# Kernel optimization log

Hardware: AMD Instinct MI355X
Metric: run time of the kernel (lower is better)

The kernel has to match this reference:

```python
import jax, jax.numpy as jnp
import numpy as np

MAX_SH_DEGREE = 3
NUM_BASES = (MAX_SH_DEGREE + 1) ** 2  # 16


def eval_sh_bases_fast(dirs):
    """SH bases up to degree 3 for unit directions [..., 3] -> [..., 16].
    Matches gsplat's _eval_sh_bases_fast constants/order."""
    x, y, z = dirs[..., 0], dirs[..., 1], dirs[..., 2]
    z2 = z * z
    fTmp0B = -1.092548430592079 * z
    fC1 = x * x - y * y
    fS1 = 2.0 * x * y
    fTmp0C = -2.285228997322329 * z2 + 0.4570457994644658
    fTmp1B = 1.445305721320277 * z
    fC2 = x * fC1 - y * fS1
    fS2 = x * fS1 + y * fC1
    ones = jnp.full_like(x, 0.2820947917738781)
    return jnp.stack([
        ones,
        -0.48860251190292 * y,
        0.48860251190292 * z,
        -0.48860251190292 * x,
        0.5462742152960395 * fS1,
        fTmp0B * y,
        0.9461746957575601 * z2 - 0.3153915652525201,
        fTmp0B * x,
        0.5462742152960395 * fC1,
        -0.5900435899266435 * fS2,
        fTmp1B * fS1,
        fTmp0C * y,
        z * (1.865881662950577 * z2 - 1.119528997770346),
        fTmp0C * x,
        fTmp1B * fC1,
        -0.5900435899266435 * fC2,
    ], axis=-1)


def setup_inputs() -> dict:
    key = jax.random.key(0)
    ks = jax.random.split(key, 10)
    C, N, F, E, W = 4, 250000, 32, 16, 128
    D_IN = E + F + NUM_BASES  # 64
    return {
        "features": jax.random.normal(ks[0], (N, F), jnp.float32),
        "dirs": jax.random.normal(ks[1], (C, N, 3), jnp.float32),
        "embed_table": jax.random.normal(ks[2], (1000, E), jnp.float32) * 0.1,
        "W0": jax.random.normal(ks[3], (D_IN, W), jnp.float32) / np.sqrt(D_IN),
        "b0": jax.random.normal(ks[4], (W,), jnp.float32) * 0.01,
        "W1": jax.random.normal(ks[5], (W, W), jnp.float32) / np.sqrt(W),
        "b1": jax.random.normal(ks[6], (W,), jnp.float32) * 0.01,
        "W2": jax.random.normal(ks[7], (W, 3), jnp.float32) / np.sqrt(W),
        "b2": jax.random.normal(ks[8], (3,), jnp.float32) * 0.01,
        "embed_ids": jax.random.randint(ks[9], (C,), 0, 1000, jnp.int64 if jax.config.jax_enable_x64 else jnp.int32),
        "sh_degree": 3,
    }


def reference(features, dirs, embed_table, W0, b0, W1, b1, W2, b2, embed_ids, sh_degree):
    C, N = dirs.shape[:2]
    E = embed_table.shape[1]
    F_dim = features.shape[1]
    # camera embeddings broadcast over splats
    emb = embed_table[embed_ids]                                   # [C, E]
    emb = jnp.broadcast_to(emb[:, None, :], (C, N, E))
    feats = jnp.broadcast_to(features[None, :, :], (C, N, F_dim))
    # F.normalize(dirs, dim=-1): divide by norm clamped at eps=1e-12
    norm = jnp.linalg.norm(dirs, axis=-1, keepdims=True)
    nd = dirs / jnp.maximum(norm, 1e-12)
    nb_use = (sh_degree + 1) ** 2  # static python int
    sh = eval_sh_bases_fast(nd)                                    # [C, N, 16]
    if nb_use < NUM_BASES:  # zero bases beyond requested degree
        mask = (jnp.arange(NUM_BASES) < nb_use).astype(sh.dtype)
        sh = sh * mask
    x = jnp.concatenate([emb, feats, sh], axis=-1)                 # [C, N, 64]
    h = jax.nn.relu(x @ W0 + b0)
    h = jax.nn.relu(h @ W1 + b1)
    return h @ W2 + b2                                             # [C, N, 3]
```

## Files before the change

kernel.cpp:

```cpp
#include <hip/hip_runtime.h>
#include <cstdint>
#include <cstddef>

typedef _Float16 half8 __attribute__((ext_vector_type(8)));
typedef __fp16 fp16x2 __attribute__((ext_vector_type(2)));
typedef float floatx16 __attribute__((ext_vector_type(16)));
typedef unsigned uint2v __attribute__((ext_vector_type(2)));


__global__ void vdc_prep_kernel(const float* __restrict__ W0,
                                const float* __restrict__ W1,
                                const float* __restrict__ W2,
                                const float* __restrict__ b0,
                                const float* __restrict__ b1,
                                const float* __restrict__ emb_tab,
                                const int* __restrict__ embed_ids,
                                int C,
                                _Float16* __restrict__ ws) {
    int i = blockIdx.x * 256 + threadIdx.x;
    int w0end   = C * 6144;
    int w1end   = w0end + 16384;
    int w2end   = w1end + 4096;
    int tailend = w2end + C * 128 + 128;
    if (i < w0end) {
        int c = i / 6144, r = i - c * 6144;
        int ci = r >> 9, l = (r >> 3) & 63, ii = r & 7;
        int mt = ci / 3, ks = ci - mt * 3;
        int j  = mt * 32 + (l & 31);
        int kk = ks * 16 + (l >> 5) * 8 + ii;
        ws[i] = (_Float16)W0[(16 + kk) * 128 + j];
    } else if (i < w1end) {
        int r = i - w0end;
        int ci = r >> 9, l = (r >> 3) & 63, ii = r & 7;
        int mt = ci >> 3, ks = ci & 7;
        int j  = mt * 32 + (l & 31);
        int kk = ks * 16 + (l >> 5) * 8 + ii;
        ws[i] = (_Float16)W1[kk * 128 + j];
    } else if (i < w2end) {
        int r = i - w1end;
        int ks = r >> 9, l = (r >> 3) & 63, ii = r & 7;
        int o  = l & 31;
        int kk = ks * 16 + (l >> 5) * 8 + ii;
        float v = 0.0f;
        if (o < 3) v = W2[kk * 3 + o];
        ws[i] = (_Float16)v;
    } else if (i < tailend) {
        int t = i - w2end;
        float* tail = (float*)(ws + w2end);
        float v;
        if (t < C * 128) {
            int c = t >> 7, j = t & 127;
            int id = embed_ids[c];
            v = b0[j];
            #pragma unroll
            for (int e = 0; e < 16; ++e)
                v += emb_tab[(size_t)id * 16 + e] * W0[e * 128 + j];
        } else {
            v = b1[t - C * 128];
        }
        tail[t] = v;
    }
}

union U4 { unsigned u[4]; half8 h; };

__device__ __forceinline__ unsigned pkr(float a, float b) {
    union { fp16x2 h; unsigned u; } x;
    x.h = __builtin_amdgcn_cvt_pkrtz(a, b);
    return x.u;
}

__device__ __forceinline__ unsigned pkrelu(float a, float b) {
    union { fp16x2 h; unsigned u; } x;
    x.h = __builtin_amdgcn_cvt_pkrtz(a, b);
    fp16x2 z = {(__fp16)0.0f, (__fp16)0.0f};
    x.h = __builtin_elementwise_max(x.h, z);
    return x.u;
}

__device__ __forceinline__ floatx16 zero16() {
    floatx16 z;
    #pragma unroll
    for (int r = 0; r < 16; ++r) z[r] = 0.0f;
    return z;
}

__device__ __forceinline__ void transition(const floatx16& a, int hl,
                                           half8& lo, half8& hi) {
    unsigned p0 = pkrelu(a[0],  a[1]);
    unsigned p1 = pkrelu(a[2],  a[3]);
    unsigned p2 = pkrelu(a[4],  a[5]);
    unsigned p3 = pkrelu(a[6],  a[7]);
    unsigned p4 = pkrelu(a[8],  a[9]);
    unsigned p5 = pkrelu(a[10], a[11]);
    unsigned p6 = pkrelu(a[12], a[13]);
    unsigned p7 = pkrelu(a[14], a[15]);
    U4 L, H;
#if __has_builtin(__builtin_amdgcn_permlane32_swap)
    uint2v s02 = __builtin_amdgcn_permlane32_swap(p0, p2, false, false);
    uint2v s13 = __builtin_amdgcn_permlane32_swap(p1, p3, false, false);
    uint2v s46 = __builtin_amdgcn_permlane32_swap(p4, p6, false, false);
    uint2v s57 = __builtin_amdgcn_permlane32_swap(p5, p7, false, false);
    L.u[0] = s02[0]; L.u[1] = s13[0]; L.u[2] = s02[1]; L.u[3] = s13[1];
    H.u[0] = s46[0]; H.u[1] = s57[0]; H.u[2] = s46[1]; H.u[3] = s57[1];
    (void)hl;
#else
    unsigned r0 = __shfl_xor(hl ? p0 : p2, 32);
    unsigned r1 = __shfl_xor(hl ? p1 : p3, 32);
    unsigned r2 = __shfl_xor(hl ? p4 : p6, 32);
    unsigned r3 = __shfl_xor(hl ? p5 : p7, 32);
    L.u[0] = hl ? r0 : p0;
    L.u[1] = hl ? r1 : p1;
    L.u[2] = hl ? p2 : r0;
    L.u[3] = hl ? p3 : r1;
    H.u[0] = hl ? r2 : p4;
    H.u[1] = hl ? r3 : p5;
    H.u[2] = hl ? p6 : r2;
    H.u[3] = hl ? p7 : r3;
#endif
    lo = L.h; hi = H.h;
}

__device__ __forceinline__ void build_bfrags(
    const float* __restrict__ feats, const float* __restrict__ dirs,
    size_t cN, int n, int hl, int nbu,
    half8& o0, half8& o1, half8& o2)
{
    const float* fp = feats + (size_t)n * 32 + hl * 8;
    float4 f0 = *(const float4*)(fp);
    float4 f1 = *(const float4*)(fp + 4);
    float4 f2 = *(const float4*)(fp + 16);
    float4 f3 = *(const float4*)(fp + 20);
    U4 u0, u1;
    u0.u[0] = pkr(f0.x, f0.y); u0.u[1] = pkr(f0.z, f0.w);
    u0.u[2] = pkr(f1.x, f1.y); u0.u[3] = pkr(f1.z, f1.w);
    u1.u[0] = pkr(f2.x, f2.y); u1.u[1] = pkr(f2.z, f2.w);
    u1.u[2] = pkr(f3.x, f3.y); u1.u[3] = pkr(f3.z, f3.w);
    o0 = u0.h; o1 = u1.h;

    const float* dp = dirs + (cN + n) * 3;
    float dx = dp[0], dy = dp[1], dz = dp[2];
    float nrm = sqrtf(dx * dx + dy * dy + dz * dz);
    float inv = 1.0f / fmaxf(nrm, 1e-12f);
    float x = dx * inv, y = dy * inv, z = dz * inv;

    float z2     = z * z;
    float fTmp0B = -1.092548430592079f * z;
    float fC1    = x * x - y * y;
    float fS1    = 2.0f * x * y;
    float fTmp0C = -2.285228997322329f * z2 + 0.4570457994644658f;
    float fTmp1B = 1.445305721320277f * z;
    float fC2    = x * fC1 - y * fS1;
    float fS2    = x * fS1 + y * fC1;

    float sh[16];
    sh[0]  = 0.2820947917738781f;
    sh[1]  = -0.48860251190292f * y;
    sh[2]  = 0.48860251190292f * z;
    sh[3]  = -0.48860251190292f * x;
    sh[4]  = 0.5462742152960395f * fS1;
    sh[5]  = fTmp0B * y;
    sh[6]  = 0.9461746957575601f * z2 - 0.3153915652525201f;
    sh[7]  = fTmp0B * x;
    sh[8]  = 0.5462742152960395f * fC1;
    sh[9]  = -0.5900435899266435f * fS2;
    sh[10] = fTmp1B * fS1;
    sh[11] = fTmp0C * y;
    sh[12] = z * (1.865881662950577f * z2 - 1.119528997770346f);
    sh[13] = fTmp0C * x;
    sh[14] = fTmp1B * fC1;
    sh[15] = -0.5900435899266435f * fC2;
    #pragma unroll
    for (int i = 0; i < 16; ++i) if (i >= nbu) sh[i] = 0.0f;

    float s0 = hl ? sh[8]  : sh[0];
    float s1 = hl ? sh[9]  : sh[1];
    float s2 = hl ? sh[10] : sh[2];
    float s3 = hl ? sh[11] : sh[3];
    float s4 = hl ? sh[12] : sh[4];
    float s5 = hl ? sh[13] : sh[5];
    float s6 = hl ? sh[14] : sh[6];
    float s7 = hl ? sh[15] : sh[7];
    U4 u2;
    u2.u[0] = pkr(s0, s1); u2.u[1] = pkr(s2, s3);
    u2.u[2] = pkr(s4, s5); u2.u[3] = pkr(s6, s7);
    o2 = u2.h;
}

#define MFMA(a, b, c) __builtin_amdgcn_mfma_f32_32x32x16_f16((a), (b), (c), 0, 0, 0)
#define LDF(off) (*(const half8*)(fr + (off)))
#define GW2(ch) (*(const half8*)(w2p + (ch) * 512 + lane * 8))

#define INIT_CB(DST, TAILOFF, MT)                                        \
    do {                                                                 \
        const float4* bp_ = (const float4*)(lds + (TAILOFF)) + (MT) * 8 + hl; \
        union { float4 f4[4]; floatx16 x; } ci_;                         \
        ci_.f4[0] = bp_[0]; ci_.f4[1] = bp_[2];                          \
        ci_.f4[2] = bp_[4]; ci_.f4[3] = bp_[6];                          \
        DST = ci_.x;                                                     \
    } while (0)

#define L0_MT(MT, HA0, HA1, HB0, HB1)                                    \
    do {                                                                 \
        floatx16 ca, cb;                                                 \
        INIT_CB(ca, 45056, MT);                                          \
        INIT_CB(cb, 45056, MT);                                          \
        half8 t0 = LDF(((MT) * 3 + 0) * 1024);                           \
        ca = MFMA(t0, ax0, ca); cb = MFMA(t0, bx0, cb);                  \
        half8 t1 = LDF(((MT) * 3 + 1) * 1024);                           \
        ca = MFMA(t1, ax1, ca); cb = MFMA(t1, bx1, cb);                  \
        half8 t2 = LDF(((MT) * 3 + 2) * 1024);                           \
        ca = MFMA(t2, ax2, ca); cb = MFMA(t2, bx2, cb);                  \
        transition(ca, hl, HA0, HA1);                                    \
        transition(cb, hl, HB0, HB1);                                    \
    } while (0)

#define L1_KS(MT, KS, HA, HB)                                            \
    do {                                                                 \
        half8 q = LDF(12288 + ((MT) * 8 + (KS)) * 1024);                 \
        ca = MFMA(q, HA, ca); cb = MFMA(q, HB, cb);                      \
    } while (0)

#define L1_MT(MT)                                                        \
    do {                                                                 \
        floatx16 ca, cb;                                                 \
        INIT_CB(ca, 45568, MT);                                          \
        INIT_CB(cb, 45568, MT);                                          \
        L1_KS(MT, 0, ha0, hb0);                                          \
        L1_KS(MT, 1, ha1, hb1);                                          \
        L1_KS(MT, 2, ha2, hb2);                                          \
        L1_KS(MT, 3, ha3, hb3);                                          \
        L1_KS(MT, 4, ha4, hb4);                                          \
        L1_KS(MT, 5, ha5, hb5);                                          \
        L1_KS(MT, 6, ha6, hb6);                                          \
        L1_KS(MT, 7, ha7, hb7);                                          \
        half8 w2a = GW2(2 * (MT) + 0);                                   \
        half8 w2b = GW2(2 * (MT) + 1);                                   \
        half8 g0, g1;                                                    \
        transition(ca, hl, g0, g1);                                      \
        acc3a = MFMA(w2a, g0, acc3a); acc3a = MFMA(w2b, g1, acc3a);      \
        transition(cb, hl, g0, g1);                                      \
        acc3b = MFMA(w2a, g0, acc3b); acc3b = MFMA(w2b, g1, acc3b);      \
    } while (0)

__global__ __launch_bounds__(256, 3) void vdc_mlp_kernel(
    const float* __restrict__ feats,
    const float* __restrict__ dirs,
    const int* __restrict__ sh_deg_p,
    const _Float16* __restrict__ ws,
    const float* __restrict__ b2p,
    float* __restrict__ out,
    int N, int C)
{
    __shared__ uint4 arena[2880];
    char* lds = (char*)arena;

    const int tid   = threadIdx.x;
    const int c     = blockIdx.y;
    const int w     = tid >> 6;
    const int lane  = tid & 63;
    const int ln    = lane & 31;
    const int hl    = lane >> 5;
    const int base  = blockIdx.x * 256 + w * 64;

    const _Float16* w2p = ws + (size_t)C * 6144 + 16384;

    {
        const uint4* srcA = (const uint4*)(ws + (size_t)c * 6144);
        const uint4* srcB = (const uint4*)(ws + (size_t)C * 6144);
        const float* tail = (const float*)(ws + (size_t)C * 6144 + 20480);
        const uint4* srcC = (const uint4*)(tail + (size_t)c * 128);
        const uint4* srcD = (const uint4*)(tail + (size_t)C * 128);
        #pragma unroll
        for (int it = 0; it < 12; ++it) {
            int idx = it * 256 + tid;
            if (idx < 2880) {
                const uint4* p;
                if (idx < 768)       p = srcA + idx;
                else if (idx < 2816) p = srcB + (idx - 768);
                else if (idx < 2848) p = srcC + (idx - 2816);
                else                 p = srcD + (idx - 2848);
                arena[idx] = *p;
            }
        }
    }

    int deg = sh_deg_p[0];
    int nbu = (deg + 1) * (deg + 1);
    float b20 = b2p[0], b21 = b2p[1], b22 = b2p[2];
    int na = base + ln;      if (na >= N) na = N - 1;
    int nb = base + 32 + ln; if (nb >= N) nb = N - 1;
    half8 ax0, ax1, ax2, bx0, bx1, bx2;
    build_bfrags(feats, dirs, (size_t)c * N, na, hl, nbu, ax0, ax1, ax2);
    build_bfrags(feats, dirs, (size_t)c * N, nb, hl, nbu, bx0, bx1, bx2);

    __syncthreads();

    const char* fr = lds + lane * 16;

    half8 ha0, ha1, ha2, ha3, ha4, ha5, ha6, ha7;
    half8 hb0, hb1, hb2, hb3, hb4, hb5, hb6, hb7;
    L0_MT(0, ha0, ha1, hb0, hb1);
    L0_MT(1, ha2, ha3, hb2, hb3);
    L0_MT(2, ha4, ha5, hb4, hb5);
    L0_MT(3, ha6, ha7, hb6, hb7);

    floatx16 acc3a = zero16();
    floatx16 acc3b = zero16();
    L1_MT(0);
    L1_MT(1);
    L1_MT(2);
    L1_MT(3);

    if (hl == 0) {
        int nn = base + ln;
        if (nn < N) {
            float* op = out + ((size_t)c * N + nn) * 3;
            op[0] = acc3a[0] + b20;
            op[1] = acc3a[1] + b21;
            op[2] = acc3a[2] + b22;
        }
        nn = base + 32 + ln;
        if (nn < N) {
            float* op = out + ((size_t)c * N + nn) * 3;
            op[0] = acc3b[0] + b20;
            op[1] = acc3b[1] + b21;
            op[2] = acc3b[2] + b22;
        }
    }
}

extern "C" void kernel_launch(void* const* d_in, const int* in_sizes, int n_in,
                              void* d_out, int out_size, void* d_ws, size_t ws_size,
                              hipStream_t stream) {
    const float* feats   = (const float*)d_in[0];
    const float* dirs    = (const float*)d_in[1];
    const float* emb_tab = (const float*)d_in[2];
    const float* W0      = (const float*)d_in[3];
    const float* b0      = (const float*)d_in[4];
    const float* W1      = (const float*)d_in[5];
    const float* b1      = (const float*)d_in[6];
    const float* W2      = (const float*)d_in[7];
    const float* b2      = (const float*)d_in[8];
    const int*   eids    = (const int*)d_in[9];
    const int*   shd     = (const int*)d_in[10];
    float* outp          = (float*)d_out;

    int N = in_sizes[0] / 32;
    int C = in_sizes[9];

    _Float16* wsh = (_Float16*)d_ws;

    int ws_threads = C * 6144 + 20480 + C * 128 + 128;
    vdc_prep_kernel<<<(ws_threads + 255) / 256, 256, 0, stream>>>(
        W0, W1, W2, b0, b1, emb_tab, eids, C, wsh);

    dim3 grid((N + 255) / 256, C);
    vdc_mlp_kernel<<<grid, 256, 0, stream>>>(
        feats, dirs, shd, wsh, b2, outp, N, C);
}
```

Baseline: 148.1 us.

## Read layer-0 weights and bias from global memory, defer LDS barrier past layer 0

Layer-0 weight fragments and per-camera bias are now loaded straight from global memory (L2-cached) instead of being staged in LDS. Only the W1 weights and b1 bias still go to shared memory, and the __syncthreads moves after the layer-0 MFMAs, so that compute overlaps the LDS staging. The bias initialisation is also shared between the two accumulators. LDS use drops from about 46KB to 33KB, which may raise occupancy. The cost is extra global-load latency on layer 0.

```diff
diff --git a/kernel.cpp b/kernel.cpp
--- a/kernel.cpp
+++ b/kernel.cpp
@@ -189,11 +189,12 @@
 
 #define MFMA(a, b, c) __builtin_amdgcn_mfma_f32_32x32x16_f16((a), (b), (c), 0, 0, 0)
 #define LDF(off) (*(const half8*)(fr + (off)))
+#define GW0(ch) (*(const half8*)(w0p + (ch) * 512 + lane * 8))
 #define GW2(ch) (*(const half8*)(w2p + (ch) * 512 + lane * 8))
 
-#define INIT_CB(DST, TAILOFF, MT)                                        \
+#define INIT_BIAS(DST, BASEF4, MT)                                       \
     do {                                                                 \
-        const float4* bp_ = (const float4*)(lds + (TAILOFF)) + (MT) * 8 + hl; \
+        const float4* bp_ = (BASEF4) + (MT) * 8 + hl;                    \
         union { float4 f4[4]; floatx16 x; } ci_;                         \
         ci_.f4[0] = bp_[0]; ci_.f4[1] = bp_[2];                          \
         ci_.f4[2] = bp_[4]; ci_.f4[3] = bp_[6];                          \
@@ -202,14 +203,14 @@
 
 #define L0_MT(MT, HA0, HA1, HB0, HB1)                                    \
     do {                                                                 \
-        floatx16 ca, cb;                                                 \
-        INIT_CB(ca, 45056, MT);                                          \
-        INIT_CB(cb, 45056, MT);                                          \
-        half8 t0 = LDF(((MT) * 3 + 0) * 1024);                           \
-        ca = MFMA(t0, ax0, ca); cb = MFMA(t0, bx0, cb);                  \
-        half8 t1 = LDF(((MT) * 3 + 1) * 1024);                           \
+        half8 t0 = GW0((MT) * 3 + 0);                                    \
+        half8 t1 = GW0((MT) * 3 + 1);                                    \
+        half8 t2 = GW0((MT) * 3 + 2);                                    \
+        floatx16 ci;                                                     \
+        INIT_BIAS(ci, cbf4, MT);                                         \
+        floatx16 ca = MFMA(t0, ax0, ci);                                 \
+        floatx16 cb = MFMA(t0, bx0, ci);                                 \
         ca = MFMA(t1, ax1, ca); cb = MFMA(t1, bx1, cb);                  \
-        half8 t2 = LDF(((MT) * 3 + 2) * 1024);                           \
         ca = MFMA(t2, ax2, ca); cb = MFMA(t2, bx2, cb);                  \
         transition(ca, hl, HA0, HA1);                                    \
         transition(cb, hl, HB0, HB1);                                    \
@@ -217,16 +218,17 @@
 
 #define L1_KS(MT, KS, HA, HB)                                            \
     do {                                                                 \
-        half8 q = LDF(12288 + ((MT) * 8 + (KS)) * 1024);                 \
+        half8 q = LDF(((MT) * 8 + (KS)) * 1024);                         \
         ca = MFMA(q, HA, ca); cb = MFMA(q, HB, cb);                      \
     } while (0)
 
 #define L1_MT(MT)                                                        \
     do {                                                                 \
-        floatx16 ca, cb;                                                 \
-        INIT_CB(ca, 45568, MT);                                          \
-        INIT_CB(cb, 45568, MT);                                          \
-        L1_KS(MT, 0, ha0, hb0);                                          \
+        floatx16 bi;                                                     \
+        INIT_BIAS(bi, b1f4, MT);                                         \
+        half8 q0 = LDF(((MT) * 8 + 0) * 1024);                           \
+        floatx16 ca = MFMA(q0, ha0, bi);                                 \
+        floatx16 cb = MFMA(q0, hb0, bi);                                 \
         L1_KS(MT, 1, ha1, hb1);                                          \
         L1_KS(MT, 2, ha2, hb2);                                          \
         L1_KS(MT, 3, ha3, hb3);                                          \
@@ -252,7 +254,7 @@
     float* __restrict__ out,
     int N, int C)
 {
-    __shared__ uint4 arena[2880];
+    __shared__ uint4 arena[2080];
     char* lds = (char*)arena;
 
     const int tid   = threadIdx.x;
@@ -263,26 +265,18 @@
     const int hl    = lane >> 5;
     const int base  = blockIdx.x * 256 + w * 64;
 
+    const _Float16* w0p = ws + (size_t)c * 6144;
     const _Float16* w2p = ws + (size_t)C * 6144 + 16384;
+    const float*   tailf = (const float*)(ws + (size_t)C * 6144 + 20480);
+    const float4*  cbf4  = (const float4*)(tailf + (size_t)c * 128);
 
     {
-        const uint4* srcA = (const uint4*)(ws + (size_t)c * 6144);
         const uint4* srcB = (const uint4*)(ws + (size_t)C * 6144);
-        const float* tail = (const float*)(ws + (size_t)C * 6144 + 20480);
-        const uint4* srcC = (const uint4*)(tail + (size_t)c * 128);
-        const uint4* srcD = (const uint4*)(tail + (size_t)C * 128);
+        const uint4* srcD = (const uint4*)(tailf + (size_t)C * 128);
         #pragma unroll
-        for (int it = 0; it < 12; ++it) {
-            int idx = it * 256 + tid;
-            if (idx < 2880) {
-                const uint4* p;
-                if (idx < 768)       p = srcA + idx;
-                else if (idx < 2816) p = srcB + (idx - 768);
-                else if (idx < 2848) p = srcC + (idx - 2816);
-                else                 p = srcD + (idx - 2848);
-                arena[idx] = *p;
-            }
-        }
+        for (int it = 0; it < 8; ++it)
+            arena[it * 256 + tid] = srcB[it * 256 + tid];
+        if (tid < 32) arena[2048 + tid] = srcD[tid];
     }
 
     int deg = sh_deg_p[0];
@@ -294,16 +288,17 @@
     build_bfrags(feats, dirs, (size_t)c * N, na, hl, nbu, ax0, ax1, ax2);
     build_bfrags(feats, dirs, (size_t)c * N, nb, hl, nbu, bx0, bx1, bx2);
 
-    __syncthreads();
-
-    const char* fr = lds + lane * 16;
-
     half8 ha0, ha1, ha2, ha3, ha4, ha5, ha6, ha7;
     half8 hb0, hb1, hb2, hb3, hb4, hb5, hb6, hb7;
     L0_MT(0, ha0, ha1, hb0, hb1);
     L0_MT(1, ha2, ha3, hb2, hb3);
     L0_MT(2, ha4, ha5, hb4, hb5);
     L0_MT(3, ha6, ha7, hb6, hb7);
+
+    __syncthreads();
+
+    const char* fr = lds + lane * 16;
+    const float4* b1f4 = (const float4*)(lds + 32768);
 
     floatx16 acc3a = zero16();
     floatx16 acc3b = zero16();
```

Measured after the change: 148.1 us. About the same (+0.0%).

## Loop each block over two chunks to amortize LDS weight staging

Applied to the files above, without the earlier changes.

The MLP kernel becomes a grid-stride loop in which each block handles about two 256-splat chunks, so the per-block copy of weights and biases into LDS is paid about half as often. Bias accumulator init is now loaded once and shared between the two MFMA chains, and the SH masking loop is skipped when every basis is in use. The cost is half as many blocks, which can mean less parallelism, and the next chunk's input loads are not overlapped with the current chunk's compute.

```diff
diff --git a/kernel.cpp b/kernel.cpp
--- a/kernel.cpp
+++ b/kernel.cpp
@@ -170,8 +170,10 @@
     sh[13] = fTmp0C * x;
     sh[14] = fTmp1B * fC1;
     sh[15] = -0.5900435899266435f * fC2;
-    #pragma unroll
-    for (int i = 0; i < 16; ++i) if (i >= nbu) sh[i] = 0.0f;
+    if (nbu < 16) {
+        #pragma unroll
+        for (int i = 0; i < 16; ++i) if (i >= nbu) sh[i] = 0.0f;
+    }
 
     float s0 = hl ? sh[8]  : sh[0];
     float s1 = hl ? sh[9]  : sh[1];
@@ -202,11 +204,11 @@
 
 #define L0_MT(MT, HA0, HA1, HB0, HB1)                                    \
     do {                                                                 \
-        floatx16 ca, cb;                                                 \
-        INIT_CB(ca, 45056, MT);                                          \
-        INIT_CB(cb, 45056, MT);                                          \
+        floatx16 ci;                                                     \
+        INIT_CB(ci, 45056, MT);                                          \
         half8 t0 = LDF(((MT) * 3 + 0) * 1024);                           \
-        ca = MFMA(t0, ax0, ca); cb = MFMA(t0, bx0, cb);                  \
+        floatx16 ca = MFMA(t0, ax0, ci);                                 \
+        floatx16 cb = MFMA(t0, bx0, ci);                                 \
         half8 t1 = LDF(((MT) * 3 + 1) * 1024);                           \
         ca = MFMA(t1, ax1, ca); cb = MFMA(t1, bx1, cb);                  \
         half8 t2 = LDF(((MT) * 3 + 2) * 1024);                           \
@@ -223,10 +225,11 @@
 
 #define L1_MT(MT)                                                        \
     do {                                                                 \
-        floatx16 ca, cb;                                                 \
-        INIT_CB(ca, 45568, MT);                                          \
-        INIT_CB(cb, 45568, MT);                                          \
-        L1_KS(MT, 0, ha0, hb0);                                          \
+        floatx16 bi;                                                     \
+        INIT_CB(bi, 45568, MT);                                          \
+        half8 q0 = LDF(12288 + ((MT) * 8 + 0) * 1024);                   \
+        floatx16 ca = MFMA(q0, ha0, bi);                                 \
+        floatx16 cb = MFMA(q0, hb0, bi);                                 \
         L1_KS(MT, 1, ha1, hb1);                                          \
         L1_KS(MT, 2, ha2, hb2);                                          \
         L1_KS(MT, 3, ha3, hb3);                                          \
@@ -250,7 +253,7 @@
     const _Float16* __restrict__ ws,
     const float* __restrict__ b2p,
     float* __restrict__ out,
-    int N, int C)
+    int N, int C, int nchunk)
 {
     __shared__ uint4 arena[2880];
     char* lds = (char*)arena;
@@ -261,7 +264,6 @@
     const int lane  = tid & 63;
     const int ln    = lane & 31;
     const int hl    = lane >> 5;
-    const int base  = blockIdx.x * 256 + w * 64;
 
     const _Float16* w2p = ws + (size_t)C * 6144 + 16384;
 
@@ -288,44 +290,65 @@
     int deg = sh_deg_p[0];
     int nbu = (deg + 1) * (deg + 1);
     float b20 = b2p[0], b21 = b2p[1], b22 = b2p[2];
-    int na = base + ln;      if (na >= N) na = N - 1;
-    int nb = base + 32 + ln; if (nb >= N) nb = N - 1;
+    const size_t cN = (size_t)c * N;
+
+    int chunk = blockIdx.x;
     half8 ax0, ax1, ax2, bx0, bx1, bx2;
-    build_bfrags(feats, dirs, (size_t)c * N, na, hl, nbu, ax0, ax1, ax2);
-    build_bfrags(feats, dirs, (size_t)c * N, nb, hl, nbu, bx0, bx1, bx2);
+    {
+        int base = chunk * 256 + w * 64;
+        int na = base + ln;      if (na >= N) na = N - 1;
+        int nb = base + 32 + ln; if (nb >= N) nb = N - 1;
+        build_bfrags(feats, dirs, cN, na, hl, nbu, ax0, ax1, ax2);
+        build_bfrags(feats, dirs, cN, nb, hl, nbu, bx0, bx1, bx2);
+    }
 
     __syncthreads();
 
     const char* fr = lds + lane * 16;
 
-    half8 ha0, ha1, ha2, ha3, ha4, ha5, ha6, ha7;
-    half8 hb0, hb1, hb2, hb3, hb4, hb5, hb6, hb7;
-    L0_MT(0, ha0, ha1, hb0, hb1);
-    L0_MT(1, ha2, ha3, hb2, hb3);
-    L0_MT(2, ha4, ha5, hb4, hb5);
-    L0_MT(3, ha6, ha7, hb6, hb7);
-
-    floatx16 acc3a = zero16();
-    floatx16 acc3b = zero16();
-    L1_MT(0);
-    L1_MT(1);
-    L1_MT(2);
-    L1_MT(3);
-
-    if (hl == 0) {
-        int nn = base + ln;
-        if (nn < N) {
-            float* op = out + ((size_t)c * N + nn) * 3;
-            op[0] = acc3a[0] + b20;
-            op[1] = acc3a[1] + b21;
-            op[2] = acc3a[2] + b22;
+    for (;;) {
+        const int base = chunk * 256 + w * 64;
+
+        half8 ha0, ha1, ha2, ha3, ha4, ha5, ha6, ha7;
+        half8 hb0, hb1, hb2, hb3, hb4, hb5, hb6, hb7;
+        L0_MT(0, ha0, ha1, hb0, hb1);
+        L0_MT(1, ha2, ha3, hb2, hb3);
+        L0_MT(2, ha4, ha5, hb4, hb5);
+        L0_MT(3, ha6, ha7, hb6, hb7);
+
+        floatx16 acc3a = zero16();
+        floatx16 acc3b = zero16();
+        L1_MT(0);
+        L1_MT(1);
+        L1_MT(2);
+        L1_MT(3);
+
+        if (hl == 0) {
+            int nn = base + ln;
+            if (nn < N) {
+                float* op = out + (cN + nn) * 3;
+                op[0] = acc3a[0] + b20;
+                op[1] = acc3a[1] + b21;
+                op[2] = acc3a[2] + b22;
+            }
+            nn = base + 32 + ln;
+            if (nn < N) {
+                float* op = out + (cN + nn) * 3;
+                op[0] = acc3b[0] + b20;
+                op[1] = acc3b[1] + b21;
+                op[2] = acc3b[2] + b22;
+            }
         }
-        nn = base + 32 + ln;
-        if (nn < N) {
-            float* op = out + ((size_t)c * N + nn) * 3;
-            op[0] = acc3b[0] + b20;
-            op[1] = acc3b[1] + b21;
-            op[2] = acc3b[2] + b22;
+
+        chunk += gridDim.x;
+        if (chunk >= nchunk) break;
+
+        {
+            int nbase = chunk * 256 + w * 64;
+            int na = nbase + ln;      if (na >= N) na = N - 1;
+            int nb = nbase + 32 + ln; if (nb >= N) nb = N - 1;
+            build_bfrags(feats, dirs, cN, na, hl, nbu, ax0, ax1, ax2);
+            build_bfrags(feats, dirs, cN, nb, hl, nbu, bx0, bx1, bx2);
         }
     }
 }
@@ -355,7 +378,10 @@
     vdc_prep_kernel<<<(ws_threads + 255) / 256, 256, 0, stream>>>(
         W0, W1, W2, b0, b1, emb_tab, eids, C, wsh);
 
-    dim3 grid((N + 255) / 256, C);
+    int nchunk = (N + 255) / 256;
+    int gx = (nchunk + 1) / 2;
+    if (gx < 1) gx = 1;
+    dim3 grid(gx, C);
     vdc_mlp_kernel<<<grid, 256, 0, stream>>>(
-        feats, dirs, shd, wsh, b2, outp, N, C);
-}
+        feats, dirs, shd, wsh, b2, outp, N, C, nchunk);
+}
```

Result: slower. 510.6 us (+244.9%).
